# Performance work log

Measured on AMD Instinct MI355X. Metric: run time of the kernel, lower is better.

Reference implementation:

```python
import jax, jax.numpy as jnp
import numpy as np
from jax import lax

D_STATE = 16
D_CONV = 4
D_MODEL = 1024
D_INNER = 2048
DT_RANK = 64
SEQLEN = 2048
BATCH = 2


def setup_inputs() -> dict:
    key = jax.random.key(0)
    ks = jax.random.split(key, 8)
    hidden_states = jax.random.normal(ks[0], (SEQLEN, BATCH, D_MODEL), jnp.float32)
    W_in = jax.random.normal(ks[1], (2 * D_INNER, D_MODEL), jnp.float32) * (D_MODEL ** -0.5)
    conv_w = jax.random.normal(ks[2], (D_INNER, D_CONV), jnp.float32) * (D_CONV ** -0.5)
    conv_b = jnp.zeros((D_INNER,), jnp.float32)
    W_x = jax.random.normal(ks[3], (DT_RANK + 2 * D_STATE, D_INNER), jnp.float32) * (D_INNER ** -0.5)
    dt_init_std = DT_RANK ** -0.5
    W_dt = jax.random.uniform(ks[4], (D_INNER, DT_RANK), jnp.float32, -dt_init_std, dt_init_std)
    # dt bias init: inverse-softplus of dt ~ LogUniform(1e-3, 1e-1)
    dt = jnp.exp(jax.random.uniform(ks[5], (D_INNER,), jnp.float32) * (np.log(0.1) - np.log(0.001)) + np.log(0.001))
    dt = jnp.clip(dt, 1e-4, None)
    dt_bias = dt + jnp.log(-jnp.expm1(-dt))
    A_log = jnp.log(jnp.tile(jnp.arange(1, D_STATE + 1, dtype=jnp.float32)[None, :], (D_INNER, 1)))
    Dp = jnp.ones((D_INNER,), jnp.float32)
    W_out = jax.random.normal(ks[6], (D_MODEL, D_INNER), jnp.float32) * (D_INNER ** -0.5)
    return {"hidden_states": hidden_states, "W_in": W_in, "conv_w": conv_w, "conv_b": conv_b,
            "W_x": W_x, "W_dt": W_dt, "dt_bias": dt_bias, "A_log": A_log, "D": Dp, "W_out": W_out}


def _mamba_forward(hidden_states, W_in, conv_w, conv_b, W_x, W_dt, dt_bias, A_log, D, W_out):
    L, B, _ = hidden_states.shape
    d_inner, d_state = A_log.shape
    dt_rank = W_dt.shape[1]
    # in_proj: [L,B,D] -> [L,B,2*d_inner] -> [B,2*d_inner,L]
    xz = jnp.einsum('lbd,ed->lbe', hidden_states, W_in)
    xz = jnp.transpose(xz, (1, 2, 0))
    x, z = jnp.split(xz, 2, axis=1)  # each [B,d_inner,L]
    # causal depthwise conv1d + silu
    x = lax.conv_general_dilated(x, conv_w[:, None, :], (1,), [(D_CONV - 1, 0)],
                                 dimension_numbers=('NCH', 'OIH', 'NCH'),
                                 feature_group_count=d_inner)
    x = jax.nn.silu(x + conv_b[None, :, None])  # [B,d_inner,L]
    # x_proj over (b l) tokens
    x_bl = jnp.transpose(x, (0, 2, 1)).reshape(B * L, d_inner)  # (b l) d
    x_dbl = x_bl @ W_x.T  # [(b l), dt_rank + 2*d_state]
    dt_lr, Bm, Cm = jnp.split(x_dbl, [dt_rank, dt_rank + d_state], axis=-1)
    dt = (W_dt @ dt_lr.T).reshape(d_inner, B, L).transpose(1, 0, 2)  # [B,d_inner,L]
    Bm = Bm.reshape(B, L, d_state)  # [B,L,n]
    Cm = Cm.reshape(B, L, d_state)
    # selective scan (delta_softplus=True, delta_bias=dt_bias)
    A = -jnp.exp(A_log)  # [d_inner, n]
    delta = jax.nn.softplus(dt + dt_bias[None, :, None])  # [B,d,L]
    delta_t = jnp.transpose(delta, (2, 0, 1))  # [L,B,d]
    u_t = jnp.transpose(x, (2, 0, 1))          # [L,B,d]
    B_t = jnp.transpose(Bm, (1, 0, 2))         # [L,B,n]
    C_t = jnp.transpose(Cm, (1, 0, 2))         # [L,B,n]

    def step(state, inp):
        d_i, u_i, b_i, c_i = inp
        dA = jnp.exp(d_i[:, :, None] * A[None])           # [B,d,n]
        dBu = (d_i * u_i)[:, :, None] * b_i[:, None, :]   # [B,d,n]
        state = state * dA + dBu
        y = jnp.einsum('bdn,bn->bd', state, c_i)
        return state, y

    init = jnp.zeros((B, d_inner, d_state), delta.dtype)
    _, ys = lax.scan(step, init, (delta_t, u_t, B_t, C_t))  # ys [L,B,d]
    y = jnp.transpose(ys, (1, 0, 2))                         # [B,L,d]
    y = y + jnp.transpose(x, (0, 2, 1)) * D[None, None, :]
    y = y * jax.nn.silu(jnp.transpose(z, (0, 2, 1)))
    out = y @ W_out.T  # [B,L,d_model]
    return jnp.transpose(out, (1, 0, 2))  # [L,B,d_model]


def reference(hidden_states, W_in, conv_w, conv_b, W_x, W_dt, dt_bias, A_log, D, W_out):
    return _mamba_forward(hidden_states, W_in, conv_w, conv_b, W_x, W_dt, dt_bias, A_log, D, W_out)
```

## Files before the change

kernel.cpp:

```cpp
#include <hip/hip_runtime.h>
#include <hip/hip_bf16.h>


#define L_SEQ 2048
#define N_B   2
#define D_M   1024
#define D_I   2048
#define D_ST  16
#define R_DT  64
#define CHNK  32
#define CT    64
#define KS    8
#define DUS   68

using bf16 = __hip_bfloat16;
typedef unsigned short u16;
typedef unsigned int u32;
typedef u16 u16x8 __attribute__((ext_vector_type(8)));
typedef __bf16 bf16x8 __attribute__((ext_vector_type(8)));
typedef float f32x4 __attribute__((ext_vector_type(4)));

__device__ __forceinline__ float b2f(u16 u) {
    union { u32 i; float f; } x;
    x.i = ((u32)u) << 16;
    return x.f;
}
__device__ __forceinline__ u16 f2b(float f) {
    union { bf16 h; u16 s; } x;
    x.h = __float2bfloat16(f);
    return x.s;
}

__device__ __forceinline__ void load4(const float* p, float* o) {
    const float4 v = *(const float4*)p;
    o[0] = v.x; o[1] = v.y; o[2] = v.z; o[3] = v.w;
}
__device__ __forceinline__ void load4(const bf16* p, float* o) {
    const ushort4 v = *(const ushort4*)(const void*)p;
    o[0] = b2f(v.x); o[1] = b2f(v.y); o[2] = b2f(v.z); o[3] = b2f(v.w);
}

__device__ __forceinline__ float softplus_f(float x) {
    return (x > 20.f) ? x : log1pf(__expf(x));
}
__device__ __forceinline__ float silu_f(float x) {
    return x / (1.f + __expf(-x));
}

__device__ __forceinline__ void gl_lds16(const u16* g, u16* l) {
    __builtin_amdgcn_global_load_lds(
        (const __attribute__((address_space(1))) void*)g,
        (__attribute__((address_space(3))) void*)l, 16, 0, 0);
}

template <int EPI>
__global__ __launch_bounds__(256) void bgemm(
    const u16* __restrict__ A, int lda,
    const u16* __restrict__ Wb, int ldb, int K,
    u16* __restrict__ bd, float* __restrict__ fout,
    const float* __restrict__ bias)
{
    __shared__ u16 As[128 * 32];
    __shared__ u16 Bs[128 * 32];

    const int tid = threadIdx.x;
    const int m0 = blockIdx.x * 128;
    const int n0 = blockIdx.y * 128;
    const int w  = tid >> 6;
    const int ln = tid & 63;

    const int sr0 = (w << 4) + (ln >> 2);
    const int sr1 = sr0 + 64;
    const int sx  = ln & 3;
    const int qa0 = (sx - (sr0 >> 1)) & 3;
    const int qa1 = (sx - (sr1 >> 1)) & 3;

    const u16* ga0 = A  + (size_t)(m0 + sr0) * lda + qa0 * 8;
    const u16* ga1 = A  + (size_t)(m0 + sr1) * lda + qa1 * 8;
    const u16* gb0 = Wb + (size_t)(n0 + sr0) * ldb + qa0 * 8;
    const u16* gb1 = Wb + (size_t)(n0 + sr1) * ldb + qa1 * 8;
    u16* la0 = As + ((w << 4) + 0) * 32;
    u16* la1 = As + ((w << 4) + 64) * 32;
    u16* lb0 = Bs + ((w << 4) + 0) * 32;
    u16* lb1 = Bs + ((w << 4) + 64) * 32;

    const int wr = (w >> 1) << 6;
    const int wc = (w & 1) << 6;
    const int lm = ln & 15;
    const int qf = ln >> 4;
    int aoff[4], boff[4];
#pragma unroll
    for (int i = 0; i < 4; ++i) {
        const int ra = wr + i * 16 + lm;
        aoff[i] = ra * 32 + (((qf + (ra >> 1)) & 3) << 3);
        const int rb = wc + i * 16 + lm;
        boff[i] = rb * 32 + (((qf + (rb >> 1)) & 3) << 3);
    }

    f32x4 acc[4][4] = {};

    for (int k0 = 0; k0 < K; k0 += 32) {
        if (k0) __syncthreads();
        gl_lds16(ga0 + k0, la0);
        gl_lds16(ga1 + k0, la1);
        gl_lds16(gb0 + k0, lb0);
        gl_lds16(gb1 + k0, lb1);
        __syncthreads();

        bf16x8 af[4], bf[4];
#pragma unroll
        for (int i = 0; i < 4; ++i) af[i] = *(const bf16x8*)&As[aoff[i]];
#pragma unroll
        for (int j = 0; j < 4; ++j) bf[j] = *(const bf16x8*)&Bs[boff[j]];
#pragma unroll
        for (int i = 0; i < 4; ++i)
#pragma unroll
            for (int j = 0; j < 4; ++j)
                acc[i][j] = __builtin_amdgcn_mfma_f32_16x16x32_bf16(
                    af[i], bf[j], acc[i][j], 0, 0, 0);
    }

    const int qr = (ln >> 4) << 2;
    float bv[4];
    if (EPI == 2) {
#pragma unroll
        for (int j = 0; j < 4; ++j) bv[j] = bias[n0 + wc + j * 16 + lm];
    }
#pragma unroll
    for (int i = 0; i < 4; ++i) {
#pragma unroll
        for (int reg = 0; reg < 4; ++reg) {
            const int rg = m0 + wr + i * 16 + qr + reg;
            if (EPI == 0) {
                const int bb = rg & (N_B - 1);
                const int l = rg >> 1;
                const size_t t = (size_t)bb * L_SEQ + l;
#pragma unroll
                for (int j = 0; j < 4; ++j)
                    bd[t * D_I + n0 + wc + j * 16 + lm] = f2b(acc[i][j][reg]);
            } else if (EPI == 1) {
                const int bb = rg >> 11;
                const int l = rg & (L_SEQ - 1);
                const size_t o = ((size_t)l * N_B + bb) * D_M;
#pragma unroll
                for (int j = 0; j < 4; ++j)
                    fout[o + n0 + wc + j * 16 + lm] = acc[i][j][reg];
            } else {
                const size_t t = (size_t)rg;
#pragma unroll
                for (int j = 0; j < 4; ++j)
                    bd[t * D_I + n0 + wc + j * 16 + lm] =
                        f2b(softplus_f(acc[i][j][reg] + bv[j]));
            }
        }
    }
}

__global__ __launch_bounds__(256) void xproj_k(
    const u16* __restrict__ u, const u16* __restrict__ Wxb,
    float* __restrict__ Part)
{
    __shared__ u16 As[64 * 32];
    __shared__ u16 Bs[96 * 264];

    const int tid = threadIdx.x;
    const int m0 = blockIdx.x * 64;
    const int kc = blockIdx.y;
    const int kbase = kc * 256;

    for (int e = tid; e < 96 * 32; e += 256) {
        const int row = e >> 5, kq = e & 31;
        const u16x8 v = *(const u16x8*)(Wxb + (size_t)row * D_I + kbase + kq * 8);
        *(u16x8*)&Bs[row * 264 + kq * 8] = v;
    }

    const int w  = tid >> 6;
    const int ln = tid & 63;
    const int sr = (w << 4) + (ln >> 2);
    const int sx = ln & 3;
    const int qa = (sx - (sr >> 1)) & 3;
    const u16* ga = u + (size_t)(m0 + sr) * D_I + kbase + qa * 8;
    u16* la = As + (w << 9);

    const int lm = ln & 15;
    const int qf = ln >> 4;
    const int ra = (w << 4) + lm;
    const int aoff = ra * 32 + (((qf + (ra >> 1)) & 3) << 3);

    f32x4 acc[6] = {};

    for (int it = 0; it < 8; ++it) {
        if (it) __syncthreads();
        gl_lds16(ga + it * 32, la);
        __syncthreads();

        const bf16x8 af = *(const bf16x8*)&As[aoff];
#pragma unroll
        for (int j = 0; j < 6; ++j) {
            const bf16x8 bf = *(const bf16x8*)&Bs[(j * 16 + lm) * 264 + it * 32 + qf * 8];
            acc[j] = __builtin_amdgcn_mfma_f32_16x16x32_bf16(af, bf, acc[j], 0, 0, 0);
        }
    }

    const int qr = (ln >> 4) << 2;
#pragma unroll
    for (int j = 0; j < 6; ++j) {
#pragma unroll
        for (int reg = 0; reg < 4; ++reg) {
            const int t = m0 + (w << 4) + qr + reg;
            Part[((size_t)kc * (N_B * L_SEQ) + t) * 96 + j * 16 + lm] = acc[j][reg];
        }
    }
}

__global__ __launch_bounds__(256) void xreduce(
    const float* __restrict__ Part, u16* __restrict__ dtlr,
    float* __restrict__ Bm, float* __restrict__ Cm)
{
    const int e = blockIdx.x * 256 + threadIdx.x;
    const int t = e / 96, c = e - t * 96;
    float s = 0.f;
#pragma unroll
    for (int kc = 0; kc < KS; ++kc)
        s += Part[(size_t)kc * (N_B * L_SEQ * 96) + e];
    if (c < 64)      dtlr[t * 64 + c] = f2b(s);
    else if (c < 80) Bm[t * 16 + (c - 64)] = s;
    else             Cm[t * 16 + (c - 80)] = s;
}

__global__ __launch_bounds__(256) void cvt_k(const float* __restrict__ s,
                                             u16* __restrict__ d)
{
    const size_t i = ((size_t)blockIdx.x * 256 + threadIdx.x) * 8;
    const float4 a = *(const float4*)(s + i);
    const float4 b = *(const float4*)(s + i + 4);
    u16 t[8] = {f2b(a.x), f2b(a.y), f2b(a.z), f2b(a.w),
                f2b(b.x), f2b(b.y), f2b(b.z), f2b(b.w)};
    *(u16x8*)(d + i) = *(const u16x8*)t;
}

__global__ __launch_bounds__(256) void gate_k(u16* __restrict__ y,
                                              const u16* __restrict__ z)
{
    const size_t i = ((size_t)blockIdx.x * 256 + threadIdx.x) * 8;
    u16x8 yv = *(u16x8*)(y + i);
    const u16x8 zv = *(const u16x8*)(z + i);
    u16 t[8];
#pragma unroll
    for (int j = 0; j < 8; ++j)
        t[j] = f2b(b2f(yv[j]) * silu_f(b2f(zv[j])));
    *(u16x8*)(y + i) = *(const u16x8*)t;
}

__global__ __launch_bounds__(256) void conv_k(
    const bf16* __restrict__ x, const float* __restrict__ cw,
    const float* __restrict__ cb, bf16* __restrict__ xc)
{
    const int t = blockIdx.x;
    const int l = t & (L_SEQ - 1);
#pragma unroll
    for (int it = 0; it < 2; ++it) {
        const int d = ((int)threadIdx.x + it * 256) << 2;
        float w[4][4], bias[4], acc[4];
#pragma unroll
        for (int dd = 0; dd < 4; ++dd)
            load4(cw + (size_t)(d + dd) * 4, w[dd]);
        load4(cb + d, bias);
#pragma unroll
        for (int dd = 0; dd < 4; ++dd) acc[dd] = bias[dd];
#pragma unroll
        for (int j = 0; j < 4; ++j) {
            const int ll = l - 3 + j;
            if (ll >= 0) {
                float xv[4];
                load4(x + (size_t)(t - 3 + j) * D_I + d, xv);
#pragma unroll
                for (int dd = 0; dd < 4; ++dd)
                    acc[dd] = fmaf(xv[dd], w[dd][j], acc[dd]);
            }
        }
        const ushort4 v = make_ushort4(f2b(silu_f(acc[0])), f2b(silu_f(acc[1])),
                                       f2b(silu_f(acc[2])), f2b(silu_f(acc[3])));
        *(ushort4*)(void*)(xc + (size_t)t * D_I + d) = v;
    }
}

template <int PHASE>
__global__ __launch_bounds__(256) void scan_chunk(
    bf16* __restrict__ dy, const bf16* __restrict__ u,
    const float* __restrict__ Bm, const float* __restrict__ Cm,
    const float* __restrict__ Alog, const float* __restrict__ Dp,
    float* __restrict__ Pc, float* __restrict__ Qc,
    const float* __restrict__ Sin)
{
    __shared__ u32 duS[CT * DUS];
    __shared__ float Bs[CT][D_ST];
    __shared__ float Cs[(PHASE == 1) ? CT : 1][D_ST];

    const int tid = threadIdx.x;
    const int d0 = blockIdx.x * 64;
    const int b  = blockIdx.y;
    const int c  = blockIdx.z;
    const int row0 = b * L_SEQ + c * CT;

    for (int e = tid; e < CT * 8; e += 256) {
        const int l = e >> 3, g = e & 7;
        const size_t go = (size_t)(row0 + l) * D_I + d0 + g * 8;
        const u16x8 d8 = *(const u16x8*)((const u16*)dy + go);
        const u16x8 u8 = *(const u16x8*)((const u16*)u + go);
        u32 w[8];
#pragma unroll
        for (int j = 0; j < 8; ++j)
            w[j] = (u32)d8[j] | ((u32)u8[j] << 16);
        *(uint4*)&duS[l * DUS + g * 8]     = make_uint4(w[0], w[1], w[2], w[3]);
        *(uint4*)&duS[l * DUS + g * 8 + 4] = make_uint4(w[4], w[5], w[6], w[7]);
    }
    {
        const float4* src = (const float4*)(Bm + (size_t)row0 * D_ST);
        float4* dst = (float4*)Bs;
        for (int e = tid; e < CT * D_ST / 4; e += 256) dst[e] = src[e];
        if (PHASE == 1) {
            const float4* s2 = (const float4*)(Cm + (size_t)row0 * D_ST);
            float4* d2 = (float4*)Cs;
            for (int e = tid; e < CT * D_ST / 4; e += 256) d2[e] = s2[e];
        }
    }
    __syncthreads();

    const int dl = tid >> 2;
    const int d  = d0 + dl;
    const int ns = tid & 3;
    const size_t pqbase = (((size_t)b * CHNK + c) * D_I + d) * D_ST + ns * 4;

    float Av[4];
    {
        const float4 a4 = *(const float4*)(Alog + (size_t)d * D_ST + ns * 4);
        Av[0] = -__expf(a4.x); Av[1] = -__expf(a4.y);
        Av[2] = -__expf(a4.z); Av[3] = -__expf(a4.w);
    }

    float st[4] = {0.f, 0.f, 0.f, 0.f};
    float P[4]  = {1.f, 1.f, 1.f, 1.f};
    if (PHASE == 1) {
        const float4 s0 = *(const float4*)(Sin + pqbase);
        st[0] = s0.x; st[1] = s0.y; st[2] = s0.z; st[3] = s0.w;
    }
    const float Dd = (PHASE == 1) ? Dp[d] : 0.f;

#pragma unroll 2
    for (int l = 0; l < CT; ++l) {
        const u32 w0 = duS[l * DUS + dl];
        union { u32 i; float f; } dvv, uvv;
        dvv.i = w0 << 16;
        uvv.i = w0 & 0xFFFF0000u;
        const float dv = dvv.f, uv = uvv.f;
        const float dvu = dv * uv;

        float bn[4], cn[4] = {0.f, 0.f, 0.f, 0.f};
        {
            const float4 b4 = *(const float4*)&Bs[l][ns * 4];
            bn[0] = b4.x; bn[1] = b4.y; bn[2] = b4.z; bn[3] = b4.w;
        }
        if (PHASE == 1) {
            const float4 c4 = *(const float4*)&Cs[l][ns * 4];
            cn[0] = c4.x; cn[1] = c4.y; cn[2] = c4.z; cn[3] = c4.w;
        }

        float y = 0.f;
#pragma unroll
        for (int j = 0; j < 4; ++j) {
            const float dA = __expf(dv * Av[j]);
            if (PHASE == 0) P[j] *= dA;
            st[j] = fmaf(st[j], dA, dvu * bn[j]);
            if (PHASE == 1) y = fmaf(st[j], cn[j], y);
        }
        if (PHASE == 1) {
            y += __shfl_xor(y, 1);
            y += __shfl_xor(y, 2);
            if (ns == 0)
                ((u16*)duS)[(l * DUS + dl) * 2] = f2b(y + uv * Dd);
        }
    }

    if (PHASE == 0) {
        *(float4*)(Pc + pqbase) = make_float4(P[0], P[1], P[2], P[3]);
        *(float4*)(Qc + pqbase) = make_float4(st[0], st[1], st[2], st[3]);
    } else {
        __syncthreads();
        for (int e = tid; e < CT * 8; e += 256) {
            const int l = e >> 3, g = e & 7;
            u16 t[8];
#pragma unroll
            for (int j = 0; j < 8; ++j)
                t[j] = (u16)(duS[l * DUS + g * 8 + j] & 0xFFFFu);
            *(u16x8*)((u16*)dy + (size_t)(row0 + l) * D_I + d0 + g * 8) =
                *(const u16x8*)t;
        }
    }
}

__global__ __launch_bounds__(256) void scan_comb(
    const float* Pc, const float* Qc, float* Sin)
{
    const int b = blockIdx.y;
    const int d = blockIdx.x * 16 + (threadIdx.x >> 4);
    const int n = threadIdx.x & 15;
    const size_t i0 = (((size_t)b * CHNK) * D_I + d) * D_ST + n;
    const size_t cs = (size_t)D_I * D_ST;

    float p[CHNK], q[CHNK];
#pragma unroll
    for (int c = 0; c < CHNK; ++c) {
        p[c] = Pc[i0 + c * cs];
        q[c] = Qc[i0 + c * cs];
    }
    float s = 0.f;
#pragma unroll
    for (int c = 0; c < CHNK; ++c) {
        Sin[i0 + c * cs] = s;
        s = fmaf(s, p[c], q[c]);
    }
}

__global__ void zfill(float* o) {
    o[(size_t)blockIdx.x * 256 + threadIdx.x] = 0.f;
}

extern "C" void kernel_launch(void* const* d_in, const int* in_sizes, int n_in,
                              void* d_out, int out_size, void* d_ws, size_t ws_size,
                              hipStream_t stream)
{
    const float* hs   = (const float*)d_in[0];
    const float* Win  = (const float*)d_in[1];
    const float* cw   = (const float*)d_in[2];
    const float* cb   = (const float*)d_in[3];
    const float* Wx   = (const float*)d_in[4];
    const float* Wdt  = (const float*)d_in[5];
    const float* dtb  = (const float*)d_in[6];
    const float* Alog = (const float*)d_in[7];
    const float* Dp   = (const float*)d_in[8];
    const float* Wout = (const float*)d_in[9];
    float* out = (float*)d_out;

    const size_t SZ = (size_t)N_B * L_SEQ * D_I;
    const size_t NT = (size_t)N_B * L_SEQ;
    const size_t NHS   = NT * D_M;
    const size_t NWIN  = (size_t)2 * D_I * D_M;
    const size_t NWOUT = (size_t)D_M * D_I;
    const size_t NWX   = (size_t)96 * D_I;
    const size_t NWDT  = (size_t)D_I * R_DT;
    const size_t NEED = SZ * 2 * sizeof(bf16)
                      + (NHS + NWIN + NWOUT + NWX + NWDT + NT * R_DT) * sizeof(u16)
                      + NT * 2 * D_ST * sizeof(float);
    if (ws_size < NEED) {
        zfill<<<dim3((unsigned)((size_t)out_size / 256)), 256, 0, stream>>>(out);
        return;
    }

    bf16* RA   = (bf16*)d_ws;
    bf16* RB   = RA + SZ;
    u16* bhs   = (u16*)(RB + SZ);
    u16* bWin  = bhs + NHS;
    u16* bWout = bWin + NWIN;
    u16* bWx   = bWout + NWOUT;
    u16* bWdt  = bWx + NWX;
    u16* dtlr  = bWdt + NWDT;
    float* Bm  = (float*)(dtlr + NT * R_DT);
    float* Cm  = Bm + NT * D_ST;
    float* Part = out;
    const size_t PQ = (size_t)N_B * CHNK * D_I * D_ST;
    float* Pc  = out;
    float* Qc  = Pc + PQ;
    float* Sin = Pc;

    cvt_k<<<dim3((unsigned)(NHS / 2048)), 256, 0, stream>>>(hs, bhs);
    cvt_k<<<dim3((unsigned)(NWIN / 2048)), 256, 0, stream>>>(Win, bWin);
    cvt_k<<<dim3((unsigned)(NWOUT / 2048)), 256, 0, stream>>>(Wout, bWout);
    cvt_k<<<dim3((unsigned)(NWX / 2048)), 256, 0, stream>>>(Wx, bWx);
    cvt_k<<<dim3((unsigned)(NWDT / 2048)), 256, 0, stream>>>(Wdt, bWdt);
    bgemm<0><<<dim3(32, 16), 256, 0, stream>>>(
        bhs, D_M, bWin, D_M, D_M, (u16*)RA, nullptr, nullptr);
    conv_k<<<dim3(N_B * L_SEQ), 256, 0, stream>>>(RA, cw, cb, RB);
    xproj_k<<<dim3(64, KS), 256, 0, stream>>>((const u16*)RB, bWx, Part);
    xreduce<<<dim3((unsigned)(NT * 96 / 256)), 256, 0, stream>>>(Part, dtlr, Bm, Cm);
    bgemm<2><<<dim3(32, 16), 256, 0, stream>>>(
        dtlr, R_DT, bWdt, R_DT, R_DT, (u16*)RA, nullptr, dtb);
    scan_chunk<0><<<dim3(D_I / 64, N_B, CHNK), 256, 0, stream>>>(
        RA, RB, Bm, Cm, Alog, Dp, Pc, Qc, nullptr);
    scan_comb<<<dim3(D_I / 16, N_B), 256, 0, stream>>>(Pc, Qc, Sin);
    scan_chunk<1><<<dim3(D_I / 64, N_B, CHNK), 256, 0, stream>>>(
        RA, RB, Bm, Cm, Alog, Dp, nullptr, nullptr, Sin);
    bgemm<0><<<dim3(32, 16), 256, 0, stream>>>(
        bhs, D_M, bWin + (size_t)D_I * D_M, D_M, D_M, (u16*)RB, nullptr, nullptr);
    gate_k<<<dim3((unsigned)(SZ / 2048)), 256, 0, stream>>>((u16*)RA, (const u16*)RB);
    bgemm<1><<<dim3(32, 8), 256, 0, stream>>>(
        (const u16*)RA, D_I, bWout, D_I, D_I, nullptr, out, nullptr);
}
```

Baseline: 358.9 us.

## Fuse gate into z-projection GEMM epilogue and streamline chunked scan

Adds a GEMM epilogue that computes the z half of the in-projection and multiplies it, through silu, into the scan output in place, so the separate gate kernel and the z buffer round trip go away. The scan kernel drops LDS padding in favour of an XOR swizzle, reads C straight from global memory with a two-step register prefetch instead of staging it in LDS, and replaces the per-step product of decay factors with a single exp of the summed delta. It also adds an occupancy hint to launch bounds. Risks are read-modify-write traffic in the GEMM epilogue and a small numerical difference from the exp-of-sum form.

```diff
diff --git a/kernel.cpp b/kernel.cpp
--- a/kernel.cpp
+++ b/kernel.cpp
@@ -11,7 +11,6 @@
 #define CHNK  32
 #define CT    64
 #define KS    8
-#define DUS   68
 
 using bf16 = __hip_bfloat16;
 typedef unsigned short u16;
@@ -145,12 +144,21 @@
 #pragma unroll
                 for (int j = 0; j < 4; ++j)
                     fout[o + n0 + wc + j * 16 + lm] = acc[i][j][reg];
-            } else {
+            } else if (EPI == 2) {
                 const size_t t = (size_t)rg;
 #pragma unroll
                 for (int j = 0; j < 4; ++j)
                     bd[t * D_I + n0 + wc + j * 16 + lm] =
                         f2b(softplus_f(acc[i][j][reg] + bv[j]));
+            } else {
+                const int bb = rg & (N_B - 1);
+                const int l = rg >> 1;
+                const size_t t = (size_t)bb * L_SEQ + l;
+#pragma unroll
+                for (int j = 0; j < 4; ++j) {
+                    u16* p = &bd[t * D_I + n0 + wc + j * 16 + lm];
+                    *p = f2b(b2f(*p) * silu_f(acc[i][j][reg]));
+                }
             }
         }
     }
@@ -239,19 +247,6 @@
     *(u16x8*)(d + i) = *(const u16x8*)t;
 }
 
-__global__ __launch_bounds__(256) void gate_k(u16* __restrict__ y,
-                                              const u16* __restrict__ z)
-{
-    const size_t i = ((size_t)blockIdx.x * 256 + threadIdx.x) * 8;
-    u16x8 yv = *(u16x8*)(y + i);
-    const u16x8 zv = *(const u16x8*)(z + i);
-    u16 t[8];
-#pragma unroll
-    for (int j = 0; j < 8; ++j)
-        t[j] = f2b(b2f(yv[j]) * silu_f(b2f(zv[j])));
-    *(u16x8*)(y + i) = *(const u16x8*)t;
-}
-
 __global__ __launch_bounds__(256) void conv_k(
     const bf16* __restrict__ x, const float* __restrict__ cw,
     const float* __restrict__ cb, bf16* __restrict__ xc)
@@ -286,16 +281,15 @@
 }
 
 template <int PHASE>
-__global__ __launch_bounds__(256) void scan_chunk(
+__global__ __launch_bounds__(256, 8) void scan_chunk(
     bf16* __restrict__ dy, const bf16* __restrict__ u,
     const float* __restrict__ Bm, const float* __restrict__ Cm,
     const float* __restrict__ Alog, const float* __restrict__ Dp,
     float* __restrict__ Pc, float* __restrict__ Qc,
     const float* __restrict__ Sin)
 {
-    __shared__ u32 duS[CT * DUS];
+    __shared__ u32 duS[CT * 64];
     __shared__ float Bs[CT][D_ST];
-    __shared__ float Cs[(PHASE == 1) ? CT : 1][D_ST];
 
     const int tid = threadIdx.x;
     const int d0 = blockIdx.x * 64;
@@ -312,18 +306,14 @@
 #pragma unroll
         for (int j = 0; j < 8; ++j)
             w[j] = (u32)d8[j] | ((u32)u8[j] << 16);
-        *(uint4*)&duS[l * DUS + g * 8]     = make_uint4(w[0], w[1], w[2], w[3]);
-        *(uint4*)&duS[l * DUS + g * 8 + 4] = make_uint4(w[4], w[5], w[6], w[7]);
+        const int c0 = (g * 8) ^ ((l & 3) << 3);
+        *(uint4*)&duS[l * 64 + c0]     = make_uint4(w[0], w[1], w[2], w[3]);
+        *(uint4*)&duS[l * 64 + c0 + 4] = make_uint4(w[4], w[5], w[6], w[7]);
     }
     {
         const float4* src = (const float4*)(Bm + (size_t)row0 * D_ST);
         float4* dst = (float4*)Bs;
         for (int e = tid; e < CT * D_ST / 4; e += 256) dst[e] = src[e];
-        if (PHASE == 1) {
-            const float4* s2 = (const float4*)(Cm + (size_t)row0 * D_ST);
-            float4* d2 = (float4*)Cs;
-            for (int e = tid; e < CT * D_ST / 4; e += 256) d2[e] = s2[e];
-        }
     }
     __syncthreads();
 
@@ -340,16 +330,24 @@
     }
 
     float st[4] = {0.f, 0.f, 0.f, 0.f};
-    float P[4]  = {1.f, 1.f, 1.f, 1.f};
+    float sdv = 0.f;
     if (PHASE == 1) {
         const float4 s0 = *(const float4*)(Sin + pqbase);
         st[0] = s0.x; st[1] = s0.y; st[2] = s0.z; st[3] = s0.w;
     }
     const float Dd = (PHASE == 1) ? Dp[d] : 0.f;
 
+    const float* Cp = Cm + (size_t)row0 * D_ST + ns * 4;
+    float4 cA, cB;
+    if (PHASE == 1) {
+        cA = *(const float4*)Cp;
+        cB = *(const float4*)(Cp + D_ST);
+    }
+
 #pragma unroll 2
     for (int l = 0; l < CT; ++l) {
-        const u32 w0 = duS[l * DUS + dl];
+        const int sw = (l & 3) << 3;
+        const u32 w0 = duS[l * 64 + (dl ^ sw)];
         union { u32 i; float f; } dvv, uvv;
         dvv.i = w0 << 16;
         uvv.i = w0 & 0xFFFF0000u;
@@ -362,15 +360,17 @@
             bn[0] = b4.x; bn[1] = b4.y; bn[2] = b4.z; bn[3] = b4.w;
         }
         if (PHASE == 1) {
-            const float4 c4 = *(const float4*)&Cs[l][ns * 4];
-            cn[0] = c4.x; cn[1] = c4.y; cn[2] = c4.z; cn[3] = c4.w;
-        }
+            cn[0] = cA.x; cn[1] = cA.y; cn[2] = cA.z; cn[3] = cA.w;
+            cA = cB;
+            if (l + 2 < CT)
+                cB = *(const float4*)(Cp + (size_t)(l + 2) * D_ST);
+        }
+        if (PHASE == 0) sdv += dv;
 
         float y = 0.f;
 #pragma unroll
         for (int j = 0; j < 4; ++j) {
             const float dA = __expf(dv * Av[j]);
-            if (PHASE == 0) P[j] *= dA;
             st[j] = fmaf(st[j], dA, dvu * bn[j]);
             if (PHASE == 1) y = fmaf(st[j], cn[j], y);
         }
@@ -378,21 +378,26 @@
             y += __shfl_xor(y, 1);
             y += __shfl_xor(y, 2);
             if (ns == 0)
-                ((u16*)duS)[(l * DUS + dl) * 2] = f2b(y + uv * Dd);
+                ((u16*)duS)[(l * 64 + (dl ^ sw)) * 2] = f2b(y + uv * Dd);
         }
     }
 
     if (PHASE == 0) {
-        *(float4*)(Pc + pqbase) = make_float4(P[0], P[1], P[2], P[3]);
+        *(float4*)(Pc + pqbase) = make_float4(
+            __expf(sdv * Av[0]), __expf(sdv * Av[1]),
+            __expf(sdv * Av[2]), __expf(sdv * Av[3]));
         *(float4*)(Qc + pqbase) = make_float4(st[0], st[1], st[2], st[3]);
     } else {
         __syncthreads();
         for (int e = tid; e < CT * 8; e += 256) {
             const int l = e >> 3, g = e & 7;
-            u16 t[8];
-#pragma unroll
-            for (int j = 0; j < 8; ++j)
-                t[j] = (u16)(duS[l * DUS + g * 8 + j] & 0xFFFFu);
+            const int c0 = (g * 8) ^ ((l & 3) << 3);
+            const uint4 a = *(const uint4*)&duS[l * 64 + c0];
+            const uint4 bq = *(const uint4*)&duS[l * 64 + c0 + 4];
+            u16 t[8] = {(u16)(a.x & 0xFFFFu),  (u16)(a.y & 0xFFFFu),
+                        (u16)(a.z & 0xFFFFu),  (u16)(a.w & 0xFFFFu),
+                        (u16)(bq.x & 0xFFFFu), (u16)(bq.y & 0xFFFFu),
+                        (u16)(bq.z & 0xFFFFu), (u16)(bq.w & 0xFFFFu)};
             *(u16x8*)((u16*)dy + (size_t)(row0 + l) * D_I + d0 + g * 8) =
                 *(const u16x8*)t;
         }
@@ -490,9 +495,8 @@
     scan_comb<<<dim3(D_I / 16, N_B), 256, 0, stream>>>(Pc, Qc, Sin);
     scan_chunk<1><<<dim3(D_I / 64, N_B, CHNK), 256, 0, stream>>>(
         RA, RB, Bm, Cm, Alog, Dp, nullptr, nullptr, Sin);
-    bgemm<0><<<dim3(32, 16), 256, 0, stream>>>(
-        bhs, D_M, bWin + (size_t)D_I * D_M, D_M, D_M, (u16*)RB, nullptr, nullptr);
-    gate_k<<<dim3((unsigned)(SZ / 2048)), 256, 0, stream>>>((u16*)RA, (const u16*)RB);
+    bgemm<3><<<dim3(32, 16), 256, 0, stream>>>(
+        bhs, D_M, bWin + (size_t)D_I * D_M, D_M, D_M, (u16*)RA, nullptr, nullptr);
     bgemm<1><<<dim3(32, 8), 256, 0, stream>>>(
         (const u16*)RA, D_I, bWout, D_I, D_I, nullptr, out, nullptr);
 }
```

New measurement: 360.6 us. No clear change (+0.5%).

## Fuse z-gate into in_proj GEMM epilogue and halve scan shared memory

Applied to the files above, without the earlier changes.

Adds a GEMM epilogue that reads the scan output y in place and multiplies it by silu(z). The z projection is never written to memory and the separate gate kernel and its memory pass are removed. The chunked scan now stages only half of each chunk in shared memory at a time, holding the second half in registers. This lowers LDS use, presumably so more blocks fit per CU. It also swaps expf for exp2 with pre-scaled A, and computes the chunk decay product as exp2 of the summed dt instead of a running product, at the cost of extra barriers and slightly different rounding.

```diff
diff --git a/kernel.cpp b/kernel.cpp
--- a/kernel.cpp
+++ b/kernel.cpp
@@ -145,12 +145,21 @@
 #pragma unroll
                 for (int j = 0; j < 4; ++j)
                     fout[o + n0 + wc + j * 16 + lm] = acc[i][j][reg];
-            } else {
+            } else if (EPI == 2) {
                 const size_t t = (size_t)rg;
 #pragma unroll
                 for (int j = 0; j < 4; ++j)
                     bd[t * D_I + n0 + wc + j * 16 + lm] =
                         f2b(softplus_f(acc[i][j][reg] + bv[j]));
+            } else {
+                const int bb = rg & (N_B - 1);
+                const int l = rg >> 1;
+                const size_t t = (size_t)bb * L_SEQ + l;
+#pragma unroll
+                for (int j = 0; j < 4; ++j) {
+                    u16* p = &bd[t * D_I + n0 + wc + j * 16 + lm];
+                    *p = f2b(b2f(*p) * silu_f(acc[i][j][reg]));
+                }
             }
         }
     }
@@ -239,19 +248,6 @@
     *(u16x8*)(d + i) = *(const u16x8*)t;
 }
 
-__global__ __launch_bounds__(256) void gate_k(u16* __restrict__ y,
-                                              const u16* __restrict__ z)
-{
-    const size_t i = ((size_t)blockIdx.x * 256 + threadIdx.x) * 8;
-    u16x8 yv = *(u16x8*)(y + i);
-    const u16x8 zv = *(const u16x8*)(z + i);
-    u16 t[8];
-#pragma unroll
-    for (int j = 0; j < 8; ++j)
-        t[j] = f2b(b2f(yv[j]) * silu_f(b2f(zv[j])));
-    *(u16x8*)(y + i) = *(const u16x8*)t;
-}
-
 __global__ __launch_bounds__(256) void conv_k(
     const bf16* __restrict__ x, const float* __restrict__ cw,
     const float* __restrict__ cb, bf16* __restrict__ xc)
@@ -293,7 +289,7 @@
     float* __restrict__ Pc, float* __restrict__ Qc,
     const float* __restrict__ Sin)
 {
-    __shared__ u32 duS[CT * DUS];
+    __shared__ u32 duS[(CT / 2) * DUS];
     __shared__ float Bs[CT][D_ST];
     __shared__ float Cs[(PHASE == 1) ? CT : 1][D_ST];
 
@@ -303,17 +299,25 @@
     const int c  = blockIdx.z;
     const int row0 = b * L_SEQ + c * CT;
 
-    for (int e = tid; e < CT * 8; e += 256) {
-        const int l = e >> 3, g = e & 7;
-        const size_t go = (size_t)(row0 + l) * D_I + d0 + g * 8;
-        const u16x8 d8 = *(const u16x8*)((const u16*)dy + go);
-        const u16x8 u8 = *(const u16x8*)((const u16*)u + go);
-        u32 w[8];
-#pragma unroll
-        for (int j = 0; j < 8; ++j)
-            w[j] = (u32)d8[j] | ((u32)u8[j] << 16);
-        *(uint4*)&duS[l * DUS + g * 8]     = make_uint4(w[0], w[1], w[2], w[3]);
-        *(uint4*)&duS[l * DUS + g * 8 + 4] = make_uint4(w[4], w[5], w[6], w[7]);
+    const int sl = tid >> 3;
+    const int sg = tid & 7;
+
+    u32 wB[8];
+    {
+        const size_t goA = (size_t)(row0 + sl) * D_I + d0 + sg * 8;
+        const size_t goB = goA + (size_t)(CT / 2) * D_I;
+        const u16x8 dA8 = *(const u16x8*)((const u16*)dy + goA);
+        const u16x8 uA8 = *(const u16x8*)((const u16*)u + goA);
+        const u16x8 dB8 = *(const u16x8*)((const u16*)dy + goB);
+        const u16x8 uB8 = *(const u16x8*)((const u16*)u + goB);
+        u32 wA[8];
+#pragma unroll
+        for (int j = 0; j < 8; ++j) {
+            wA[j] = (u32)dA8[j] | ((u32)uA8[j] << 16);
+            wB[j] = (u32)dB8[j] | ((u32)uB8[j] << 16);
+        }
+        *(uint4*)&duS[sl * DUS + sg * 8]     = make_uint4(wA[0], wA[1], wA[2], wA[3]);
+        *(uint4*)&duS[sl * DUS + sg * 8 + 4] = make_uint4(wA[4], wA[5], wA[6], wA[7]);
     }
     {
         const float4* src = (const float4*)(Bm + (size_t)row0 * D_ST);
@@ -335,67 +339,86 @@
     float Av[4];
     {
         const float4 a4 = *(const float4*)(Alog + (size_t)d * D_ST + ns * 4);
-        Av[0] = -__expf(a4.x); Av[1] = -__expf(a4.y);
-        Av[2] = -__expf(a4.z); Av[3] = -__expf(a4.w);
+        const float l2e = 1.4426950408889634f;
+        Av[0] = -__expf(a4.x) * l2e; Av[1] = -__expf(a4.y) * l2e;
+        Av[2] = -__expf(a4.z) * l2e; Av[3] = -__expf(a4.w) * l2e;
     }
 
     float st[4] = {0.f, 0.f, 0.f, 0.f};
-    float P[4]  = {1.f, 1.f, 1.f, 1.f};
+    float sdv = 0.f;
     if (PHASE == 1) {
         const float4 s0 = *(const float4*)(Sin + pqbase);
         st[0] = s0.x; st[1] = s0.y; st[2] = s0.z; st[3] = s0.w;
     }
     const float Dd = (PHASE == 1) ? Dp[d] : 0.f;
 
+#pragma unroll
+    for (int half = 0; half < 2; ++half) {
+        if (half) {
+            __syncthreads();
+            if (PHASE == 1) {
+                u16 t[8];
+#pragma unroll
+                for (int j = 0; j < 8; ++j)
+                    t[j] = (u16)(duS[sl * DUS + sg * 8 + j] & 0xFFFFu);
+                *(u16x8*)((u16*)dy + (size_t)(row0 + sl) * D_I + d0 + sg * 8) =
+                    *(const u16x8*)t;
+                __syncthreads();
+            }
+            *(uint4*)&duS[sl * DUS + sg * 8]     = make_uint4(wB[0], wB[1], wB[2], wB[3]);
+            *(uint4*)&duS[sl * DUS + sg * 8 + 4] = make_uint4(wB[4], wB[5], wB[6], wB[7]);
+            __syncthreads();
+        }
+        const int lb = half * (CT / 2);
 #pragma unroll 2
-    for (int l = 0; l < CT; ++l) {
-        const u32 w0 = duS[l * DUS + dl];
-        union { u32 i; float f; } dvv, uvv;
-        dvv.i = w0 << 16;
-        uvv.i = w0 & 0xFFFF0000u;
-        const float dv = dvv.f, uv = uvv.f;
-        const float dvu = dv * uv;
-
-        float bn[4], cn[4] = {0.f, 0.f, 0.f, 0.f};
-        {
-            const float4 b4 = *(const float4*)&Bs[l][ns * 4];
-            bn[0] = b4.x; bn[1] = b4.y; bn[2] = b4.z; bn[3] = b4.w;
-        }
-        if (PHASE == 1) {
-            const float4 c4 = *(const float4*)&Cs[l][ns * 4];
-            cn[0] = c4.x; cn[1] = c4.y; cn[2] = c4.z; cn[3] = c4.w;
-        }
-
-        float y = 0.f;
-#pragma unroll
-        for (int j = 0; j < 4; ++j) {
-            const float dA = __expf(dv * Av[j]);
-            if (PHASE == 0) P[j] *= dA;
-            st[j] = fmaf(st[j], dA, dvu * bn[j]);
-            if (PHASE == 1) y = fmaf(st[j], cn[j], y);
-        }
-        if (PHASE == 1) {
-            y += __shfl_xor(y, 1);
-            y += __shfl_xor(y, 2);
-            if (ns == 0)
-                ((u16*)duS)[(l * DUS + dl) * 2] = f2b(y + uv * Dd);
+        for (int l = 0; l < CT / 2; ++l) {
+            const u32 w0 = duS[l * DUS + dl];
+            union { u32 i; float f; } dvv, uvv;
+            dvv.i = w0 << 16;
+            uvv.i = w0 & 0xFFFF0000u;
+            const float dv = dvv.f, uv = uvv.f;
+            const float dvu = dv * uv;
+
+            float bn[4], cn[4] = {0.f, 0.f, 0.f, 0.f};
+            {
+                const float4 b4 = *(const float4*)&Bs[lb + l][ns * 4];
+                bn[0] = b4.x; bn[1] = b4.y; bn[2] = b4.z; bn[3] = b4.w;
+            }
+            if (PHASE == 1) {
+                const float4 c4 = *(const float4*)&Cs[lb + l][ns * 4];
+                cn[0] = c4.x; cn[1] = c4.y; cn[2] = c4.z; cn[3] = c4.w;
+            }
+            if (PHASE == 0) sdv += dv;
+
+            float y = 0.f;
+#pragma unroll
+            for (int j = 0; j < 4; ++j) {
+                const float dA = __builtin_amdgcn_exp2f(dv * Av[j]);
+                st[j] = fmaf(st[j], dA, dvu * bn[j]);
+                if (PHASE == 1) y = fmaf(st[j], cn[j], y);
+            }
+            if (PHASE == 1) {
+                y += __shfl_xor(y, 1);
+                y += __shfl_xor(y, 2);
+                if (ns == 0)
+                    ((u16*)duS)[(l * DUS + dl) * 2] = f2b(y + uv * Dd);
+            }
         }
     }
 
     if (PHASE == 0) {
-        *(float4*)(Pc + pqbase) = make_float4(P[0], P[1], P[2], P[3]);
+        *(float4*)(Pc + pqbase) = make_float4(
+            __builtin_amdgcn_exp2f(sdv * Av[0]), __builtin_amdgcn_exp2f(sdv * Av[1]),
+            __builtin_amdgcn_exp2f(sdv * Av[2]), __builtin_amdgcn_exp2f(sdv * Av[3]));
         *(float4*)(Qc + pqbase) = make_float4(st[0], st[1], st[2], st[3]);
     } else {
         __syncthreads();
-        for (int e = tid; e < CT * 8; e += 256) {
-            const int l = e >> 3, g = e & 7;
-            u16 t[8];
-#pragma unroll
-            for (int j = 0; j < 8; ++j)
-                t[j] = (u16)(duS[l * DUS + g * 8 + j] & 0xFFFFu);
-            *(u16x8*)((u16*)dy + (size_t)(row0 + l) * D_I + d0 + g * 8) =
-                *(const u16x8*)t;
-        }
+        u16 t[8];
+#pragma unroll
+        for (int j = 0; j < 8; ++j)
+            t[j] = (u16)(duS[sl * DUS + sg * 8 + j] & 0xFFFFu);
+        *(u16x8*)((u16*)dy + (size_t)(row0 + CT / 2 + sl) * D_I + d0 + sg * 8) =
+            *(const u16x8*)t;
     }
 }
 
@@ -490,9 +513,8 @@
     scan_comb<<<dim3(D_I / 16, N_B), 256, 0, stream>>>(Pc, Qc, Sin);
     scan_chunk<1><<<dim3(D_I / 64, N_B, CHNK), 256, 0, stream>>>(
         RA, RB, Bm, Cm, Alog, Dp, nullptr, nullptr, Sin);
-    bgemm<0><<<dim3(32, 16), 256, 0, stream>>>(
-        bhs, D_M, bWin + (size_t)D_I * D_M, D_M, D_M, (u16*)RB, nullptr, nullptr);
-    gate_k<<<dim3((unsigned)(SZ / 2048)), 256, 0, stream>>>((u16*)RA, (const u16*)RB);
+    bgemm<3><<<dim3(32, 16), 256, 0, stream>>>(
+        bhs, D_M, bWin + (size_t)D_I * D_M, D_M, D_M, (u16*)RA, nullptr, nullptr);
     bgemm<1><<<dim3(32, 8), 256, 0, stream>>>(
         (const u16*)RA, D_I, bWout, D_I, D_I, nullptr, out, nullptr);
 }
```

Result: faster. 348.1 us (-3.0%).
